# Performance work log

Measured on AMD Instinct MI355X. Metric: run time of the kernel, lower is better.

Reference implementation:

```python
import jax, jax.numpy as jnp
import numpy as np

EPS = 1e-5
DIM_HEAD = 64
HEADS = 8

def layernorm(x, gamma, beta):
    mu = jnp.mean(x, axis=-1, keepdims=True)
    var = jnp.var(x, axis=-1, keepdims=True)
    return (x - mu) * jax.lax.rsqrt(var + EPS) * gamma + beta

def setup_inputs() -> dict:
    key = jax.random.key(0)
    ks = jax.random.split(key, 8)
    b, n, dh = 1, 896, 3072       # batch, enformer seq len, enformer_hidden_dim
    c, j, dc = 64, 127, 1024      # num contexts (tracks), context len, context_dim
    inner = HEADS * DIM_HEAD      # 512
    return {
        "embeddings": jax.random.normal(ks[0], (b, n, dh), jnp.float32),
        "context": jax.random.normal(ks[1], (c, j, dc), jnp.float32),
        "context_mask": jax.random.randint(ks[2], (b, j), 0, 2) > 0,
        "q_gamma": jnp.ones((dh,), jnp.float32),
        "q_beta": jnp.zeros((dh,), jnp.float32),
        "kv_gamma": jnp.ones((dc,), jnp.float32),
        "kv_beta": jnp.zeros((dc,), jnp.float32),
        "Wq": jax.random.normal(ks[3], (dh, inner), jnp.float32) * 0.02,
        "Wkv": jax.random.normal(ks[4], (dc, 2 * inner), jnp.float32) * 0.02,
        "null_k": jax.random.normal(ks[5], (inner,), jnp.float32),
        "null_v": jax.random.normal(ks[6], (inner,), jnp.float32),
        "Wo": jax.random.normal(ks[7], (inner, dh), jnp.float32) * 0.02,
        "bo": jnp.zeros((dh,), jnp.float32),
        "Wp": jax.random.normal(jax.random.fold_in(key, 9), (dh, 1), jnp.float32) * 0.02,
        "bp": jnp.zeros((1,), jnp.float32),
    }

def reference(embeddings, context, context_mask, q_gamma, q_beta, kv_gamma, kv_beta,
              Wq, Wkv, null_k, null_v, Wo, bo, Wp, bp):
    h, d = HEADS, DIM_HEAD
    scale = d ** -0.5
    b, n, dh = embeddings.shape
    c = context.shape[0]
    # projections
    q = layernorm(embeddings, q_gamma, q_beta) @ Wq            # (b, n, h*d)
    kv = layernorm(context, kv_gamma, kv_beta) @ Wkv           # (c, j, 2*h*d)
    k, v = jnp.split(kv, 2, axis=-1)
    # prepend null key/value token
    k = jnp.concatenate([jnp.broadcast_to(null_k, (c, 1, h * d)), k], axis=1)
    v = jnp.concatenate([jnp.broadcast_to(null_v, (c, 1, h * d)), v], axis=1)
    # split heads: (b, h, i, d) / (c, h, j, d)
    q = q.reshape(b, n, h, d).transpose(0, 2, 1, 3)
    k = k.reshape(c, -1, h, d).transpose(0, 2, 1, 3)
    v = v.reshape(c, -1, h, d).transpose(0, 2, 1, 3)
    sim = jnp.einsum('bhid,chjd->bchij', q, k) * scale         # (b, c, h, i, j+1)
    # mask: pad with True for the null token, broadcast over c, h, i
    mask = jnp.pad(context_mask, ((0, 0), (1, 0)), constant_values=True)
    sim = jnp.where(mask[:, None, None, None, :], sim, -jnp.finfo(sim.dtype).max)
    attn = jax.nn.softmax(sim, axis=-1)
    out = jnp.einsum('bchij,chjd->bchid', attn, v)             # (b, c, h, i, d)
    out = out.transpose(0, 1, 3, 2, 4).reshape(b, c, n, h * d)  # (b, c, n, h*d)
    branch = out @ Wo + bo                                     # (b, c, n, dh)
    emb = embeddings[:, None] + branch                         # (b, c, n, dh)
    pred = jax.nn.softplus((emb @ Wp + bp)[..., 0])            # (b, c, n)
    return pred.transpose(0, 2, 1)                             # (b, n, c)
```

## Files before the change

kernel.cpp:

```cpp
#include <hip/hip_runtime.h>
#include <math.h>

#define N_SEQ   896
#define DH      3072
#define NCTX    64
#define JLEN    127
#define DC      1024
#define HEADS   8
#define DHEAD   64
#define INNER   512
#define MKV     8128
#define MKVPAD  8192

typedef __bf16 bf16x8 __attribute__((ext_vector_type(8)));
typedef float  f32x4  __attribute__((ext_vector_type(4)));

#define OFF_EDOT   0LL
#define OFF_QBF    (OFF_EDOT + N_SEQ)
#define OFF_KBF    (OFF_QBF  + (long long)N_SEQ*INNER/2)
#define OFF_VPM    (OFF_KBF  + (long long)NCTX*128*INNER/2)
#define OFF_VPNULL (OFF_VPM  + (long long)MKV*8)
#define OFF_WOP    (OFF_VPNULL + 8)
#define OFF_BOP    (OFF_WOP  + INNER)
#define OFF_SBUF   (OFF_BOP  + 16)
#define OFF_ANQ    (OFF_SBUF + (long long)NCTX*HEADS*N_SEQ)
#define OFF_ANKV   (OFF_ANQ  + (long long)N_SEQ*DH/2)
#define OFF_WQT    (OFF_ANKV + (long long)MKVPAD*DC/2)
#define OFF_WKT    (OFF_WQT  + (long long)INNER*DH/2)
#define OFF_WVPT   (OFF_WKT  + (long long)INNER*DC/2)
#define OFF_QSL    (OFF_WVPT + 16*1024/2)

__device__ __forceinline__ void async_copy16(const __bf16* g, __bf16* l) {
    __builtin_amdgcn_global_load_lds(
        (const __attribute__((address_space(1))) unsigned int*)g,
        (__attribute__((address_space(3))) unsigned int*)l,
        16, 0, 0);
}

template <int P>
__device__ __forceinline__
void ln_row(const float* __restrict__ x,
            const float* __restrict__ gamma, const float* __restrict__ beta,
            const float* __restrict__ wp,
            __bf16* __restrict__ o, float* __restrict__ dotout) {
    const int K = P * 1024;
    float4 xv[P];
    float s = 0.f, ss = 0.f, dp = 0.f;
    #pragma unroll
    for (int p = 0; p < P; ++p) {
        xv[p] = *(const float4*)&x[p * 1024 + threadIdx.x * 4];
        s  += xv[p].x + xv[p].y + xv[p].z + xv[p].w;
        ss += xv[p].x * xv[p].x + xv[p].y * xv[p].y
            + xv[p].z * xv[p].z + xv[p].w * xv[p].w;
        if (wp) {
            float4 w4 = *(const float4*)&wp[p * 1024 + threadIdx.x * 4];
            dp += xv[p].x * w4.x + xv[p].y * w4.y + xv[p].z * w4.z + xv[p].w * w4.w;
        }
    }
    #pragma unroll
    for (int ofs = 32; ofs > 0; ofs >>= 1) {
        s  += __shfl_down(s,  ofs);
        ss += __shfl_down(ss, ofs);
        dp += __shfl_down(dp, ofs);
    }
    __shared__ float red[3][4];
    __shared__ float sh_mu, sh_rstd;
    int lane = threadIdx.x & 63, w = threadIdx.x >> 6;
    if (lane == 0) { red[0][w] = s; red[1][w] = ss; red[2][w] = dp; }
    __syncthreads();
    if (threadIdx.x == 0) {
        float S  = red[0][0] + red[0][1] + red[0][2] + red[0][3];
        float SS = red[1][0] + red[1][1] + red[1][2] + red[1][3];
        float m = S / K;
        sh_mu = m;
        sh_rstd = rsqrtf(SS / K - m * m + 1e-5f);
        if (dotout) *dotout = red[2][0] + red[2][1] + red[2][2] + red[2][3];
    }
    __syncthreads();
    float m = sh_mu, r = sh_rstd;
    #pragma unroll
    for (int p = 0; p < P; ++p) {
        int col = p * 1024 + threadIdx.x * 4;
        float4 g4 = *(const float4*)&gamma[col];
        float4 b4 = *(const float4*)&beta[col];
        __bf16 ov[4];
        ov[0] = (__bf16)((xv[p].x - m) * r * g4.x + b4.x);
        ov[1] = (__bf16)((xv[p].y - m) * r * g4.y + b4.y);
        ov[2] = (__bf16)((xv[p].z - m) * r * g4.z + b4.z);
        ov[3] = (__bf16)((xv[p].w - m) * r * g4.w + b4.w);
        *(ushort4*)&o[col] = *(ushort4*)ov;
    }
}

__global__ __launch_bounds__(256)
void ln_wop_kernel(const float* __restrict__ emb, const float* __restrict__ ctx,
                   const float* __restrict__ qg, const float* __restrict__ qb,
                   const float* __restrict__ kvg, const float* __restrict__ kvb,
                   const float* __restrict__ Wp, const float* __restrict__ Wo,
                   const float* __restrict__ bo,
                   __bf16* __restrict__ anq, __bf16* __restrict__ ankv,
                   float* __restrict__ edot, float* __restrict__ wop,
                   float* __restrict__ bop) {
    int b = blockIdx.x;
    if (b < N_SEQ) {
        ln_row<3>(emb + (long long)b * DH, qg, qb, Wp,
                  anq + (long long)b * DH, edot + b);
    } else if (b < N_SEQ + MKV) {
        int r = b - N_SEQ;
        ln_row<1>(ctx + (long long)r * DC, kvg, kvb, nullptr,
                  ankv + (long long)r * DC, nullptr);
    } else {
        int r = b - (N_SEQ + MKV);
        const float* src = (r < INNER) ? (Wo + (long long)r * DH) : bo;
        float s = 0.f;
        for (int k = threadIdx.x; k < DH; k += 256) s += src[k] * Wp[k];
        #pragma unroll
        for (int o = 32; o > 0; o >>= 1) s += __shfl_down(s, o);
        __shared__ float red2[4];
        int lane = threadIdx.x & 63, w = threadIdx.x >> 6;
        if (lane == 0) red2[w] = s;
        __syncthreads();
        if (threadIdx.x == 0) {
            float S = red2[0] + red2[1] + red2[2] + red2[3];
            if (r < INNER) wop[r] = S; else *bop = S;
        }
    }
}

__device__ __forceinline__
void transpose_tile(const float* __restrict__ src, int srcStride,
                    __bf16* __restrict__ dst, int dstStride,
                    int rb, int cb, float t[32][33]) {
    int tx = threadIdx.x & 31, ty = threadIdx.x >> 5;
    #pragma unroll
    for (int i = 0; i < 32; i += 8)
        t[ty + i][tx] = src[(long long)(rb + ty + i) * srcStride + cb + tx];
    __syncthreads();
    #pragma unroll
    for (int i = 0; i < 32; i += 8)
        dst[(long long)(cb + ty + i) * dstStride + rb + tx] = (__bf16)t[tx][ty + i];
}

__global__ __launch_bounds__(256)
void prep2_kernel(const float* __restrict__ Wq, const float* __restrict__ Wkv,
                  const float* __restrict__ wop,
                  const float* __restrict__ null_v, const float* __restrict__ null_k,
                  __bf16* __restrict__ wqt, __bf16* __restrict__ wkt,
                  __bf16* __restrict__ wvpt, float* __restrict__ vpnull,
                  __bf16* __restrict__ k_bf) {
    __shared__ float t[32][33];
    int b = blockIdx.x;
    if (b < 1536) {
        int rb = (b >> 4) * 32, cb = (b & 15) * 32;
        transpose_tile(Wq, INNER, wqt, DH, rb, cb, t);
    } else if (b < 2048) {
        int bi = b - 1536;
        int rb = (bi >> 4) * 32, cb = (bi & 15) * 32;
        transpose_tile(Wkv, 2 * INNER, wkt, DC, rb, cb, t);
    } else if (b < 2080) {
        int tt = (b - 2048) * 256 + threadIdx.x;
        int k = tt >> 3, h = tt & 7;
        const float* src = Wkv + (long long)k * (2 * INNER) + INNER + h * 64;
        const float* wv  = wop + h * 64;
        float s = 0.f;
        #pragma unroll 16
        for (int d = 0; d < 64; ++d) s += src[d] * wv[d];
        wvpt[h * 1024 + k] = (__bf16)s;
    } else {
        for (int i = threadIdx.x; i < 8 * 1024; i += 256)
            wvpt[8 * 1024 + i] = (__bf16)0.f;
        for (int i = threadIdx.x; i < NCTX * INNER; i += 256) {
            int c = i >> 9, d = i & 511;
            k_bf[(long long)(c * 128) * INNER + d] = (__bf16)null_k[d];
        }
        if (threadIdx.x < 8) {
            int h = threadIdx.x;
            float s = 0.f;
            #pragma unroll 16
            for (int d = 0; d < 64; ++d) s += null_v[h * 64 + d] * wop[h * 64 + d];
            vpnull[h] = s;
        }
    }
}

__global__ __launch_bounds__(256)
void proj_kernel(const __bf16* __restrict__ ANQ, const __bf16* __restrict__ WQT,
                 const __bf16* __restrict__ ANKV, const __bf16* __restrict__ WKT,
                 const __bf16* __restrict__ WVPT,
                 float* __restrict__ qsl, __bf16* __restrict__ kout,
                 float* __restrict__ vpm) {
    __shared__ __align__(16) __bf16 As[128 * 32];
    __shared__ __align__(16) __bf16 Bs[128 * 32];
    int b = blockIdx.x;
    int tid = threadIdx.x;
    int lane = tid & 63, w = tid >> 6;
    int n16 = lane & 15, quad = lane >> 4;
    int wr = (w >> 1) * 64, wc = (w & 1) * 64;

    const __bf16 *A, *B;
    int K, kbeg, kend, mode, slice = 0;
    long long m0, n0;
    if (b < 224) {
        mode = 0; slice = b / 28;
        int rem = b % 28;
        m0 = (long long)(rem % 7) * 128;
        n0 = (long long)(rem / 7) * 128;
        K = DH; kbeg = slice * 384; kend = kbeg + 384;
        A = ANQ; B = WQT;
    } else {
        mode = 1;
        int b2 = b - 224;
        m0 = (long long)(b2 & 63) * 128;
        n0 = (long long)(b2 >> 6) * 128;
        K = DC; kbeg = 0; kend = DC;
        A = ANKV; B = WKT;
    }
    bool dovp = (mode == 1) && (n0 == 0);

    const __bf16* aG = A + (m0 + (tid >> 2)) * K + (tid & 3) * 8;
    const __bf16* bG = B + (n0 + (tid >> 2)) * K + (tid & 3) * 8;
    __bf16* aL = As + tid * 8;
    __bf16* bL = Bs + tid * 8;

    f32x4 acc[4][4], accv[4];
    const f32x4 z = {0.f, 0.f, 0.f, 0.f};
    #pragma unroll
    for (int i = 0; i < 4; ++i) {
        accv[i] = z;
        #pragma unroll
        for (int j = 0; j < 4; ++j) acc[i][j] = z;
    }

    for (int k0 = kbeg; k0 < kend; k0 += 32) {
        async_copy16(aG + k0, aL);
        async_copy16(aG + (long long)64 * K + k0, aL + 2048);
        async_copy16(bG + k0, bL);
        async_copy16(bG + (long long)64 * K + k0, bL + 2048);
        bf16x8 bv;
        if (dovp) bv = *(const bf16x8*)&WVPT[n16 * 1024 + k0 + quad * 8];
        __syncthreads();
        bf16x8 af[4], bfr[4];
        #pragma unroll
        for (int i = 0; i < 4; ++i)
            af[i]  = *(const bf16x8*)&As[(wr + i * 16 + n16) * 32 + quad * 8];
        #pragma unroll
        for (int j = 0; j < 4; ++j)
            bfr[j] = *(const bf16x8*)&Bs[(wc + j * 16 + n16) * 32 + quad * 8];
        #pragma unroll
        for (int i = 0; i < 4; ++i)
            #pragma unroll
            for (int j = 0; j < 4; ++j)
                acc[i][j] = __builtin_amdgcn_mfma_f32_16x16x32_bf16(af[i], bfr[j], acc[i][j], 0, 0, 0);
        if (dovp) {
            #pragma unroll
            for (int i = 0; i < 4; ++i)
                accv[i] = __builtin_amdgcn_mfma_f32_16x16x32_bf16(af[i], bv, accv[i], 0, 0, 0);
        }
        __syncthreads();
    }

    if (mode == 0) {
        float* qdst = qsl + (long long)slice * (N_SEQ * INNER);
        #pragma unroll
        for (int i = 0; i < 4; ++i)
            #pragma unroll
            for (int r = 0; r < 4; ++r) {
                long long gr = m0 + wr + i * 16 + quad * 4 + r;
                #pragma unroll
                for (int j = 0; j < 4; ++j) {
                    long long gc = n0 + wc + j * 16 + n16;
                    qdst[gr * INNER + gc] = acc[i][j][r];
                }
            }
    } else {
        #pragma unroll
        for (int i = 0; i < 4; ++i)
            #pragma unroll
            for (int r = 0; r < 4; ++r) {
                long long gr = m0 + wr + i * 16 + quad * 4 + r;
                if (gr >= MKV) continue;
                int cc = (int)(gr / JLEN), jj = (int)(gr % JLEN);
                #pragma unroll
                for (int j = 0; j < 4; ++j) {
                    long long gc = n0 + wc + j * 16 + n16;
                    kout[((long long)(cc * 128) + jj + 1) * INNER + gc] = (__bf16)acc[i][j][r];
                }
                if (dovp && n16 < 8) vpm[gr * 8 + n16] = accv[i][r];
            }
    }
}

__global__ void qreduce_kernel(const float* __restrict__ qsl, __bf16* __restrict__ qbf) {
    int t = blockIdx.x * 256 + threadIdx.x;
    float s = 0.f;
    #pragma unroll
    for (int k = 0; k < 8; ++k) s += qsl[(long long)k * (N_SEQ * INNER) + t];
    qbf[t] = (__bf16)s;
}

#define KROW 72

__global__ __launch_bounds__(256)
void attn_mfma_kernel(const __bf16* __restrict__ qb, const __bf16* __restrict__ kb,
                      const float* __restrict__ vpm, const float* __restrict__ vpnull,
                      const int* __restrict__ mask, float* __restrict__ s_buf) {
    __shared__ __align__(16) __bf16 ksh[128 * KROW];
    __shared__ float vpsh[128];
    __shared__ float amsh[128];
    int ch = blockIdx.y;
    int h = ch & 7, c = ch >> 3;
    int tid = threadIdx.x;
    int lane = tid & 63, w = tid >> 6;
    int n16 = lane & 15, quad = lane >> 4;

    const __bf16* kbase = kb + (long long)(c * 128) * INNER + h * DHEAD;
    #pragma unroll
    for (int p = 0; p < 4; ++p) {
        int chunk = tid + p * 256;
        int row = chunk >> 3, o = chunk & 7;
        bf16x8 v = *(const bf16x8*)(kbase + (long long)row * INNER + o * 8);
        *(bf16x8*)&ksh[row * KROW + o * 8] = v;
    }
    if (tid < 128) {
        vpsh[tid] = (tid == 0) ? vpnull[h] : vpm[(long long)(c * JLEN + tid - 1) * 8 + h];
        amsh[tid] = (tid == 0) ? 0.f : (mask[tid - 1] ? 0.f : -3.0e38f);
    }
    __syncthreads();

    bf16x8 bF[8][2];
    #pragma unroll
    for (int t = 0; t < 8; ++t)
        #pragma unroll
        for (int s = 0; s < 2; ++s)
            bF[t][s] = *(const bf16x8*)&ksh[(t * 16 + n16) * KROW + s * 32 + quad * 8];

    float vpv[8], am[8];
    #pragma unroll
    for (int t = 0; t < 8; ++t) {
        vpv[t] = vpsh[t * 16 + n16];
        am[t]  = amsh[t * 16 + n16];
    }

    const __bf16* qbase = qb + h * DHEAD;
    bf16x8 aF[2][2];
    int r0s[2];
    #pragma unroll
    for (int it2 = 0; it2 < 2; ++it2) {
        int tile = blockIdx.x * 8 + it2 * 4 + w;
        r0s[it2] = tile * 16;
        const __bf16* qrow = qbase + (long long)(r0s[it2] + n16) * INNER + quad * 8;
        aF[it2][0] = *(const bf16x8*)(qrow);
        aF[it2][1] = *(const bf16x8*)(qrow + 32);
    }

    const f32x4 zero = {0.f, 0.f, 0.f, 0.f};
    #pragma unroll
    for (int it2 = 0; it2 < 2; ++it2) {
        int r0 = r0s[it2];
        f32x4 acc[8];
        #pragma unroll
        for (int t = 0; t < 8; ++t) {
            acc[t] = __builtin_amdgcn_mfma_f32_16x16x32_bf16(aF[it2][0], bF[t][0], zero,   0, 0, 0);
            acc[t] = __builtin_amdgcn_mfma_f32_16x16x32_bf16(aF[it2][1], bF[t][1], acc[t], 0, 0, 0);
        }
        float mloc = -3.0e38f;
        #pragma unroll
        for (int t = 0; t < 8; ++t)
            #pragma unroll
            for (int r = 0; r < 4; ++r)
                mloc = fmaxf(mloc, acc[t][r] * 0.125f + am[t]);
        #pragma unroll
        for (int o = 1; o < 16; o <<= 1) mloc = fmaxf(mloc, __shfl_xor(mloc, o, 16));
        float lr[4] = {0.f, 0.f, 0.f, 0.f}, pr[4] = {0.f, 0.f, 0.f, 0.f};
        #pragma unroll
        for (int t = 0; t < 8; ++t) {
            #pragma unroll
            for (int r = 0; r < 4; ++r) {
                float e = __expf(acc[t][r] * 0.125f + am[t] - mloc);
                lr[r] += e; pr[r] += e * vpv[t];
            }
        }
        #pragma unroll
        for (int o = 1; o < 16; o <<= 1) {
            #pragma unroll
            for (int r = 0; r < 4; ++r) {
                lr[r] += __shfl_xor(lr[r], o, 16);
                pr[r] += __shfl_xor(pr[r], o, 16);
            }
        }
        if (n16 == 0) {
            #pragma unroll
            for (int r = 0; r < 4; ++r)
                s_buf[(long long)ch * N_SEQ + r0 + quad * 4 + r] = pr[r] / lr[r];
        }
    }
}

__global__ void final_kernel(const float* __restrict__ s_buf,
                             const float* __restrict__ e_dot,
                             const float* __restrict__ bop,
                             const float* __restrict__ bp,
                             float* __restrict__ out) {
    int t = blockIdx.x * blockDim.x + threadIdx.x;
    if (t >= N_SEQ * NCTX) return;
    int n = t >> 6, c = t & 63;
    float s = 0.f;
    #pragma unroll
    for (int h = 0; h < HEADS; ++h) s += s_buf[((long long)(c * HEADS + h)) * N_SEQ + n];
    float x = e_dot[n] + s + *bop + *bp;
    out[t] = fmaxf(x, 0.f) + log1pf(__expf(-fabsf(x)));
}

extern "C" void kernel_launch(void* const* d_in, const int* in_sizes, int n_in,
                              void* d_out, int out_size, void* d_ws, size_t ws_size,
                              hipStream_t stream) {
    const float* emb   = (const float*)d_in[0];
    const float* ctx   = (const float*)d_in[1];
    const int*   cmask = (const int*)  d_in[2];
    const float* qg    = (const float*)d_in[3];
    const float* qb_   = (const float*)d_in[4];
    const float* kvg   = (const float*)d_in[5];
    const float* kvb   = (const float*)d_in[6];
    const float* Wq    = (const float*)d_in[7];
    const float* Wkv   = (const float*)d_in[8];
    const float* nullk = (const float*)d_in[9];
    const float* nullv = (const float*)d_in[10];
    const float* Wo    = (const float*)d_in[11];
    const float* bo    = (const float*)d_in[12];
    const float* Wp    = (const float*)d_in[13];
    const float* bp    = (const float*)d_in[14];
    float* out  = (float*)d_out;
    float* ws_f = (float*)d_ws;

    float*  EDOT   = ws_f + OFF_EDOT;
    __bf16* QBF    = (__bf16*)(ws_f + OFF_QBF);
    __bf16* KBF    = (__bf16*)(ws_f + OFF_KBF);
    float*  VPM    = ws_f + OFF_VPM;
    float*  VPNULL = ws_f + OFF_VPNULL;
    float*  WOP    = ws_f + OFF_WOP;
    float*  BOP    = ws_f + OFF_BOP;
    float*  SBUF   = ws_f + OFF_SBUF;
    __bf16* ANQ    = (__bf16*)(ws_f + OFF_ANQ);
    __bf16* ANKV   = (__bf16*)(ws_f + OFF_ANKV);
    __bf16* WQT    = (__bf16*)(ws_f + OFF_WQT);
    __bf16* WKT    = (__bf16*)(ws_f + OFF_WKT);
    __bf16* WVPT   = (__bf16*)(ws_f + OFF_WVPT);
    float*  QSL    = ws_f + OFF_QSL;

    ln_wop_kernel<<<N_SEQ + MKV + INNER + 1, 256, 0, stream>>>(
        emb, ctx, qg, qb_, kvg, kvb, Wp, Wo, bo, ANQ, ANKV, EDOT, WOP, BOP);
    prep2_kernel<<<2081, 256, 0, stream>>>(
        Wq, Wkv, WOP, nullv, nullk, WQT, WKT, WVPT, VPNULL, KBF);
    proj_kernel<<<480, 256, 0, stream>>>(ANQ, WQT, ANKV, WKT, WVPT, QSL, KBF, VPM);
    qreduce_kernel<<<(N_SEQ * INNER) / 256, 256, 0, stream>>>(QSL, QBF);
    attn_mfma_kernel<<<dim3(7, NCTX * HEADS), 256, 0, stream>>>(
        QBF, KBF, VPM, VPNULL, cmask, SBUF);
    final_kernel<<<(N_SEQ * NCTX + 255) / 256, 256, 0, stream>>>(SBUF, EDOT, BOP, bp, out);
}
```

Before: 216.1 us.

## Fuse all stages into one cooperative persistent kernel with grid syncs

Replaces the six-kernel pipeline (layernorm, weight prep, projection GEMM, q-reduce, attention, final softplus) with a single cooperative kernel whose blocks loop over each stage's work and separate stages with grid-wide barriers. The layernorm becomes one wave per row instead of one block per row, and the Wo·Wp fold is merged into the per-head value-projection work. The aim is to remove kernel launch gaps and tail idle time between stages. In exchange, grid size is capped by occupancy, so some stages run with fewer concurrent blocks, and each grid sync costs time of its own.

```diff
diff --git a/kernel.cpp b/kernel.cpp
--- a/kernel.cpp
+++ b/kernel.cpp
@@ -1,5 +1,8 @@
 #include <hip/hip_runtime.h>
+#include <hip/hip_cooperative_groups.h>
 #include <math.h>
+
+namespace cg = cooperative_groups;
 
 #define N_SEQ   896
 #define DH      3072
@@ -37,378 +40,417 @@
         16, 0, 0);
 }
 
-template <int P>
-__device__ __forceinline__
-void ln_row(const float* __restrict__ x,
-            const float* __restrict__ gamma, const float* __restrict__ beta,
-            const float* __restrict__ wp,
-            __bf16* __restrict__ o, float* __restrict__ dotout) {
-    const int K = P * 1024;
-    float4 xv[P];
-    float s = 0.f, ss = 0.f, dp = 0.f;
-    #pragma unroll
-    for (int p = 0; p < P; ++p) {
-        xv[p] = *(const float4*)&x[p * 1024 + threadIdx.x * 4];
-        s  += xv[p].x + xv[p].y + xv[p].z + xv[p].w;
-        ss += xv[p].x * xv[p].x + xv[p].y * xv[p].y
-            + xv[p].z * xv[p].z + xv[p].w * xv[p].w;
-        if (wp) {
-            float4 w4 = *(const float4*)&wp[p * 1024 + threadIdx.x * 4];
-            dp += xv[p].x * w4.x + xv[p].y * w4.y + xv[p].z * w4.z + xv[p].w * w4.w;
-        }
-    }
-    #pragma unroll
-    for (int ofs = 32; ofs > 0; ofs >>= 1) {
-        s  += __shfl_down(s,  ofs);
-        ss += __shfl_down(ss, ofs);
-        dp += __shfl_down(dp, ofs);
-    }
-    __shared__ float red[3][4];
-    __shared__ float sh_mu, sh_rstd;
-    int lane = threadIdx.x & 63, w = threadIdx.x >> 6;
-    if (lane == 0) { red[0][w] = s; red[1][w] = ss; red[2][w] = dp; }
-    __syncthreads();
-    if (threadIdx.x == 0) {
-        float S  = red[0][0] + red[0][1] + red[0][2] + red[0][3];
-        float SS = red[1][0] + red[1][1] + red[1][2] + red[1][3];
-        float m = S / K;
-        sh_mu = m;
-        sh_rstd = rsqrtf(SS / K - m * m + 1e-5f);
-        if (dotout) *dotout = red[2][0] + red[2][1] + red[2][2] + red[2][3];
-    }
-    __syncthreads();
-    float m = sh_mu, r = sh_rstd;
-    #pragma unroll
-    for (int p = 0; p < P; ++p) {
-        int col = p * 1024 + threadIdx.x * 4;
-        float4 g4 = *(const float4*)&gamma[col];
-        float4 b4 = *(const float4*)&beta[col];
-        __bf16 ov[4];
-        ov[0] = (__bf16)((xv[p].x - m) * r * g4.x + b4.x);
-        ov[1] = (__bf16)((xv[p].y - m) * r * g4.y + b4.y);
-        ov[2] = (__bf16)((xv[p].z - m) * r * g4.z + b4.z);
-        ov[3] = (__bf16)((xv[p].w - m) * r * g4.w + b4.w);
-        *(ushort4*)&o[col] = *(ushort4*)ov;
-    }
-}
-
-__global__ __launch_bounds__(256)
-void ln_wop_kernel(const float* __restrict__ emb, const float* __restrict__ ctx,
-                   const float* __restrict__ qg, const float* __restrict__ qb,
-                   const float* __restrict__ kvg, const float* __restrict__ kvb,
-                   const float* __restrict__ Wp, const float* __restrict__ Wo,
-                   const float* __restrict__ bo,
-                   __bf16* __restrict__ anq, __bf16* __restrict__ ankv,
-                   float* __restrict__ edot, float* __restrict__ wop,
-                   float* __restrict__ bop) {
-    int b = blockIdx.x;
-    if (b < N_SEQ) {
-        ln_row<3>(emb + (long long)b * DH, qg, qb, Wp,
-                  anq + (long long)b * DH, edot + b);
-    } else if (b < N_SEQ + MKV) {
-        int r = b - N_SEQ;
-        ln_row<1>(ctx + (long long)r * DC, kvg, kvb, nullptr,
-                  ankv + (long long)r * DC, nullptr);
-    } else {
-        int r = b - (N_SEQ + MKV);
-        const float* src = (r < INNER) ? (Wo + (long long)r * DH) : bo;
-        float s = 0.f;
-        for (int k = threadIdx.x; k < DH; k += 256) s += src[k] * Wp[k];
-        #pragma unroll
-        for (int o = 32; o > 0; o >>= 1) s += __shfl_down(s, o);
-        __shared__ float red2[4];
-        int lane = threadIdx.x & 63, w = threadIdx.x >> 6;
-        if (lane == 0) red2[w] = s;
-        __syncthreads();
-        if (threadIdx.x == 0) {
-            float S = red2[0] + red2[1] + red2[2] + red2[3];
-            if (r < INNER) wop[r] = S; else *bop = S;
-        }
-    }
-}
-
-__device__ __forceinline__
-void transpose_tile(const float* __restrict__ src, int srcStride,
-                    __bf16* __restrict__ dst, int dstStride,
-                    int rb, int cb, float t[32][33]) {
-    int tx = threadIdx.x & 31, ty = threadIdx.x >> 5;
-    #pragma unroll
-    for (int i = 0; i < 32; i += 8)
-        t[ty + i][tx] = src[(long long)(rb + ty + i) * srcStride + cb + tx];
-    __syncthreads();
-    #pragma unroll
-    for (int i = 0; i < 32; i += 8)
-        dst[(long long)(cb + ty + i) * dstStride + rb + tx] = (__bf16)t[tx][ty + i];
-}
-
-__global__ __launch_bounds__(256)
-void prep2_kernel(const float* __restrict__ Wq, const float* __restrict__ Wkv,
-                  const float* __restrict__ wop,
-                  const float* __restrict__ null_v, const float* __restrict__ null_k,
-                  __bf16* __restrict__ wqt, __bf16* __restrict__ wkt,
-                  __bf16* __restrict__ wvpt, float* __restrict__ vpnull,
-                  __bf16* __restrict__ k_bf) {
-    __shared__ float t[32][33];
-    int b = blockIdx.x;
-    if (b < 1536) {
-        int rb = (b >> 4) * 32, cb = (b & 15) * 32;
-        transpose_tile(Wq, INNER, wqt, DH, rb, cb, t);
-    } else if (b < 2048) {
-        int bi = b - 1536;
-        int rb = (bi >> 4) * 32, cb = (bi & 15) * 32;
-        transpose_tile(Wkv, 2 * INNER, wkt, DC, rb, cb, t);
-    } else if (b < 2080) {
-        int tt = (b - 2048) * 256 + threadIdx.x;
-        int k = tt >> 3, h = tt & 7;
-        const float* src = Wkv + (long long)k * (2 * INNER) + INNER + h * 64;
-        const float* wv  = wop + h * 64;
-        float s = 0.f;
-        #pragma unroll 16
-        for (int d = 0; d < 64; ++d) s += src[d] * wv[d];
-        wvpt[h * 1024 + k] = (__bf16)s;
-    } else {
-        for (int i = threadIdx.x; i < 8 * 1024; i += 256)
-            wvpt[8 * 1024 + i] = (__bf16)0.f;
-        for (int i = threadIdx.x; i < NCTX * INNER; i += 256) {
-            int c = i >> 9, d = i & 511;
-            k_bf[(long long)(c * 128) * INNER + d] = (__bf16)null_k[d];
-        }
-        if (threadIdx.x < 8) {
-            int h = threadIdx.x;
+#define KROW 72
+
+__global__ __launch_bounds__(256, 2)
+void mega_kernel(const float* __restrict__ emb, const float* __restrict__ ctx,
+                 const int* __restrict__ cmask,
+                 const float* __restrict__ qg, const float* __restrict__ qb_,
+                 const float* __restrict__ kvg, const float* __restrict__ kvb,
+                 const float* __restrict__ Wq, const float* __restrict__ Wkv,
+                 const float* __restrict__ nullk, const float* __restrict__ nullv,
+                 const float* __restrict__ Wo, const float* __restrict__ bo,
+                 const float* __restrict__ Wp, const float* __restrict__ bp,
+                 float* __restrict__ out, float* __restrict__ ws_f)
+{
+    __shared__ __align__(16) unsigned char SMEM[19456];
+    cg::grid_group gg = cg::this_grid();
+
+    float*  EDOT   = ws_f + OFF_EDOT;
+    __bf16* QBF    = (__bf16*)(ws_f + OFF_QBF);
+    __bf16* KBF    = (__bf16*)(ws_f + OFF_KBF);
+    float*  VPM    = ws_f + OFF_VPM;
+    float*  VPNULL = ws_f + OFF_VPNULL;
+    float*  BOP    = ws_f + OFF_BOP;
+    float*  SBUF   = ws_f + OFF_SBUF;
+    __bf16* ANQ    = (__bf16*)(ws_f + OFF_ANQ);
+    __bf16* ANKV   = (__bf16*)(ws_f + OFF_ANKV);
+    __bf16* WQT    = (__bf16*)(ws_f + OFF_WQT);
+    __bf16* WKT    = (__bf16*)(ws_f + OFF_WKT);
+    __bf16* WVPT   = (__bf16*)(ws_f + OFF_WVPT);
+    float*  QSL    = ws_f + OFF_QSL;
+
+    const int NB   = gridDim.x;
+    const int bid  = blockIdx.x;
+    const int tid  = threadIdx.x;
+    const int lane = tid & 63;
+    const int wid  = tid >> 6;
+
+    {
+        const int gw = bid * 4 + wid, NW = NB * 4;
+        for (int r = gw; r < MKV; r += NW) {
+            const float* x = ctx + (long long)r * DC;
+            float4 xv[4];
+            float s = 0.f, ss = 0.f;
+            #pragma unroll
+            for (int c = 0; c < 4; ++c) {
+                xv[c] = *(const float4*)&x[c * 256 + lane * 4];
+                s  += xv[c].x + xv[c].y + xv[c].z + xv[c].w;
+                ss += xv[c].x*xv[c].x + xv[c].y*xv[c].y + xv[c].z*xv[c].z + xv[c].w*xv[c].w;
+            }
+            #pragma unroll
+            for (int o = 1; o < 64; o <<= 1) { s += __shfl_xor(s, o); ss += __shfl_xor(ss, o); }
+            float m = s * (1.f / DC);
+            float rs = rsqrtf(ss * (1.f / DC) - m * m + 1e-5f);
+            __bf16* op = ANKV + (long long)r * DC;
+            #pragma unroll
+            for (int c = 0; c < 4; ++c) {
+                int col = c * 256 + lane * 4;
+                float4 g4 = *(const float4*)&kvg[col];
+                float4 b4 = *(const float4*)&kvb[col];
+                __bf16 ov[4];
+                ov[0] = (__bf16)((xv[c].x - m) * rs * g4.x + b4.x);
+                ov[1] = (__bf16)((xv[c].y - m) * rs * g4.y + b4.y);
+                ov[2] = (__bf16)((xv[c].z - m) * rs * g4.z + b4.z);
+                ov[3] = (__bf16)((xv[c].w - m) * rs * g4.w + b4.w);
+                *(ushort4*)&op[col] = *(ushort4*)ov;
+            }
+        }
+        for (int r = gw; r < N_SEQ; r += NW) {
+            const float* x = emb + (long long)r * DH;
+            float4 xv[12];
+            float s = 0.f, ss = 0.f, dp = 0.f;
+            #pragma unroll
+            for (int c = 0; c < 12; ++c) {
+                int col = c * 256 + lane * 4;
+                xv[c] = *(const float4*)&x[col];
+                float4 w4 = *(const float4*)&Wp[col];
+                s  += xv[c].x + xv[c].y + xv[c].z + xv[c].w;
+                ss += xv[c].x*xv[c].x + xv[c].y*xv[c].y + xv[c].z*xv[c].z + xv[c].w*xv[c].w;
+                dp += xv[c].x*w4.x + xv[c].y*w4.y + xv[c].z*w4.z + xv[c].w*w4.w;
+            }
+            #pragma unroll
+            for (int o = 1; o < 64; o <<= 1) {
+                s += __shfl_xor(s, o); ss += __shfl_xor(ss, o); dp += __shfl_xor(dp, o);
+            }
+            float m = s * (1.f / DH);
+            float rs = rsqrtf(ss * (1.f / DH) - m * m + 1e-5f);
+            __bf16* op = ANQ + (long long)r * DH;
+            #pragma unroll
+            for (int c = 0; c < 12; ++c) {
+                int col = c * 256 + lane * 4;
+                float4 g4 = *(const float4*)&qg[col];
+                float4 b4 = *(const float4*)&qb_[col];
+                __bf16 ov[4];
+                ov[0] = (__bf16)((xv[c].x - m) * rs * g4.x + b4.x);
+                ov[1] = (__bf16)((xv[c].y - m) * rs * g4.y + b4.y);
+                ov[2] = (__bf16)((xv[c].z - m) * rs * g4.z + b4.z);
+                ov[3] = (__bf16)((xv[c].w - m) * rs * g4.w + b4.w);
+                *(ushort4*)&op[col] = *(ushort4*)ov;
+            }
+            if (lane == 0) EDOT[r] = dp;
+        }
+    }
+
+    {
+        float (*tT)[33] = (float(*)[33])SMEM;
+        for (int t = bid; t < 2058; t += NB) {
+            if (t < 2048) {
+                const float* src; __bf16* dst; int srcS, dstS, rb, cb;
+                if (t < 1536) {
+                    rb = (t >> 4) * 32; cb = (t & 15) * 32;
+                    src = Wq; srcS = INNER; dst = WQT; dstS = DH;
+                } else {
+                    int bi = t - 1536;
+                    rb = (bi >> 4) * 32; cb = (bi & 15) * 32;
+                    src = Wkv; srcS = 2 * INNER; dst = WKT; dstS = DC;
+                }
+                int tx = tid & 31, ty = tid >> 5;
+                __syncthreads();
+                #pragma unroll
+                for (int i = 0; i < 32; i += 8)
+                    tT[ty + i][tx] = src[(long long)(rb + ty + i) * srcS + cb + tx];
+                __syncthreads();
+                #pragma unroll
+                for (int i = 0; i < 32; i += 8)
+                    dst[(long long)(cb + ty + i) * dstS + rb + tx] = (__bf16)tT[tx][ty + i];
+            } else if (t < 2056) {
+                int h = t - 2048;
+                float* wops = (float*)SMEM;
+                __syncthreads();
+                int d = tid >> 2, part = tid & 3;
+                const float* worow = Wo + (long long)(h * 64 + d) * DH;
+                float s = 0.f;
+                for (int k = part * 4; k < DH; k += 16) {
+                    float4 a = *(const float4*)&worow[k];
+                    float4 w = *(const float4*)&Wp[k];
+                    s += a.x*w.x + a.y*w.y + a.z*w.z + a.w*w.w;
+                }
+                s += __shfl_xor(s, 1); s += __shfl_xor(s, 2);
+                if (part == 0) wops[d] = s;
+                __syncthreads();
+                if (tid < 64) {
+                    float v = nullv[h * 64 + tid] * wops[tid];
+                    #pragma unroll
+                    for (int o = 1; o < 64; o <<= 1) v += __shfl_xor(v, o);
+                    if (tid == 0) VPNULL[h] = v;
+                }
+                for (int k = tid; k < 1024; k += 256) {
+                    const float* src = Wkv + (long long)k * (2 * INNER) + INNER + h * 64;
+                    float s2 = 0.f;
+                    #pragma unroll
+                    for (int d2 = 0; d2 < 64; d2 += 4) {
+                        float4 a = *(const float4*)&src[d2];
+                        s2 += a.x*wops[d2] + a.y*wops[d2+1] + a.z*wops[d2+2] + a.w*wops[d2+3];
+                    }
+                    WVPT[h * 1024 + k] = (__bf16)s2;
+                }
+            } else if (t == 2056) {
+                float* red = (float*)SMEM;
+                __syncthreads();
+                float s = 0.f;
+                #pragma unroll
+                for (int i = 0; i < 3; ++i) {
+                    int k = i * 1024 + tid * 4;
+                    float4 a = *(const float4*)&bo[k];
+                    float4 w = *(const float4*)&Wp[k];
+                    s += a.x*w.x + a.y*w.y + a.z*w.z + a.w*w.w;
+                }
+                #pragma unroll
+                for (int o = 1; o < 64; o <<= 1) s += __shfl_xor(s, o);
+                if (lane == 0) red[wid] = s;
+                __syncthreads();
+                if (tid == 0) *BOP = red[0] + red[1] + red[2] + red[3];
+            } else {
+                for (int i = tid; i < 8 * 1024; i += 256)
+                    WVPT[8 * 1024 + i] = (__bf16)0.f;
+                for (int i = tid; i < NCTX * INNER; i += 256) {
+                    int c = i >> 9, d2 = i & 511;
+                    KBF[(long long)(c * 128) * INNER + d2] = (__bf16)nullk[d2];
+                }
+            }
+        }
+    }
+
+    gg.sync();
+
+    {
+        __bf16* As = (__bf16*)SMEM;
+        __bf16* Bs = As + 128 * 32;
+        for (int b = bid; b < 480; b += NB) {
+            int n16 = lane & 15, quad = lane >> 4;
+            int wr = (wid >> 1) * 64, wc = (wid & 1) * 64;
+
+            const __bf16 *A, *B;
+            int K, kbeg, kend, mode, slice = 0;
+            long long m0, n0;
+            if (b < 224) {
+                mode = 0; slice = b / 28;
+                int rem = b % 28;
+                m0 = (long long)(rem % 7) * 128;
+                n0 = (long long)(rem / 7) * 128;
+                K = DH; kbeg = slice * 384; kend = kbeg + 384;
+                A = ANQ; B = WQT;
+            } else {
+                mode = 1;
+                int b2 = b - 224;
+                m0 = (long long)(b2 & 63) * 128;
+                n0 = (long long)(b2 >> 6) * 128;
+                K = DC; kbeg = 0; kend = DC;
+                A = ANKV; B = WKT;
+            }
+            bool dovp = (mode == 1) && (n0 == 0);
+
+            const __bf16* aG = A + (m0 + (tid >> 2)) * K + (tid & 3) * 8;
+            const __bf16* bG = B + (n0 + (tid >> 2)) * K + (tid & 3) * 8;
+            __bf16* aL = As + tid * 8;
+            __bf16* bL = Bs + tid * 8;
+
+            f32x4 acc[4][4], accv[4];
+            const f32x4 z = {0.f, 0.f, 0.f, 0.f};
+            #pragma unroll
+            for (int i = 0; i < 4; ++i) {
+                accv[i] = z;
+                #pragma unroll
+                for (int j = 0; j < 4; ++j) acc[i][j] = z;
+            }
+
+            for (int k0 = kbeg; k0 < kend; k0 += 32) {
+                async_copy16(aG + k0, aL);
+                async_copy16(aG + (long long)64 * K + k0, aL + 2048);
+                async_copy16(bG + k0, bL);
+                async_copy16(bG + (long long)64 * K + k0, bL + 2048);
+                bf16x8 bv;
+                if (dovp) bv = *(const bf16x8*)&WVPT[n16 * 1024 + k0 + quad * 8];
+                __syncthreads();
+                bf16x8 af[4], bfr[4];
+                #pragma unroll
+                for (int i = 0; i < 4; ++i)
+                    af[i]  = *(const bf16x8*)&As[(wr + i * 16 + n16) * 32 + quad * 8];
+                #pragma unroll
+                for (int j = 0; j < 4; ++j)
+                    bfr[j] = *(const bf16x8*)&Bs[(wc + j * 16 + n16) * 32 + quad * 8];
+                #pragma unroll
+                for (int i = 0; i < 4; ++i)
+                    #pragma unroll
+                    for (int j = 0; j < 4; ++j)
+                        acc[i][j] = __builtin_amdgcn_mfma_f32_16x16x32_bf16(af[i], bfr[j], acc[i][j], 0, 0, 0);
+                if (dovp) {
+                    #pragma unroll
+                    for (int i = 0; i < 4; ++i)
+                        accv[i] = __builtin_amdgcn_mfma_f32_16x16x32_bf16(af[i], bv, accv[i], 0, 0, 0);
+                }
+                __syncthreads();
+            }
+
+            if (mode == 0) {
+                float* qdst = QSL + (long long)slice * (N_SEQ * INNER);
+                #pragma unroll
+                for (int i = 0; i < 4; ++i)
+                    #pragma unroll
+                    for (int r = 0; r < 4; ++r) {
+                        long long gr = m0 + wr + i * 16 + quad * 4 + r;
+                        #pragma unroll
+                        for (int j = 0; j < 4; ++j) {
+                            long long gc = n0 + wc + j * 16 + n16;
+                            qdst[gr * INNER + gc] = acc[i][j][r];
+                        }
+                    }
+            } else {
+                #pragma unroll
+                for (int i = 0; i < 4; ++i)
+                    #pragma unroll
+                    for (int r = 0; r < 4; ++r) {
+                        long long gr = m0 + wr + i * 16 + quad * 4 + r;
+                        if (gr >= MKV) continue;
+                        int cc = (int)(gr / JLEN), jj = (int)(gr % JLEN);
+                        #pragma unroll
+                        for (int j = 0; j < 4; ++j) {
+                            long long gc = n0 + wc + j * 16 + n16;
+                            KBF[((long long)(cc * 128) + jj + 1) * INNER + gc] = (__bf16)acc[i][j][r];
+                        }
+                        if (dovp && n16 < 8) VPM[gr * 8 + n16] = accv[i][r];
+                    }
+            }
+        }
+    }
+
+    gg.sync();
+
+    {
+        const int gt = bid * 256 + tid, NT = NB * 256;
+        for (int i = gt; i < (N_SEQ * INNER) / 4; i += NT) {
+            float4 s4 = {0.f, 0.f, 0.f, 0.f};
+            #pragma unroll
+            for (int k = 0; k < 8; ++k) {
+                float4 a = *(const float4*)&QSL[(long long)k * (N_SEQ * INNER) + i * 4];
+                s4.x += a.x; s4.y += a.y; s4.z += a.z; s4.w += a.w;
+            }
+            __bf16 ov[4] = {(__bf16)s4.x, (__bf16)s4.y, (__bf16)s4.z, (__bf16)s4.w};
+            *(ushort4*)&QBF[i * 4] = *(ushort4*)ov;
+        }
+    }
+
+    gg.sync();
+
+    {
+        __bf16* ksh  = (__bf16*)SMEM;
+        float*  vpsh = (float*)(SMEM + 18432);
+        float*  amsh = (float*)(SMEM + 18944);
+        for (int t = bid; t < 3584; t += NB) {
+            int ch = t & 511, qx = t >> 9;
+            int h = ch & 7, c = ch >> 3;
+            int n16 = lane & 15, quad = lane >> 4;
+
+            __syncthreads();
+            const __bf16* kbase = KBF + (long long)(c * 128) * INNER + h * DHEAD;
+            #pragma unroll
+            for (int p = 0; p < 4; ++p) {
+                int chunk = tid + p * 256;
+                int row = chunk >> 3, o = chunk & 7;
+                bf16x8 v = *(const bf16x8*)(kbase + (long long)row * INNER + o * 8);
+                *(bf16x8*)&ksh[row * KROW + o * 8] = v;
+            }
+            if (tid < 128) {
+                vpsh[tid] = (tid == 0) ? VPNULL[h] : VPM[(long long)(c * JLEN + tid - 1) * 8 + h];
+                amsh[tid] = (tid == 0) ? 0.f : (cmask[tid - 1] ? 0.f : -3.0e38f);
+            }
+            __syncthreads();
+
+            bf16x8 bF[8][2];
+            #pragma unroll
+            for (int tt = 0; tt < 8; ++tt)
+                #pragma unroll
+                for (int s = 0; s < 2; ++s)
+                    bF[tt][s] = *(const bf16x8*)&ksh[(tt * 16 + n16) * KROW + s * 32 + quad * 8];
+
+            float vpv[8], am[8];
+            #pragma unroll
+            for (int tt = 0; tt < 8; ++tt) {
+                vpv[tt] = vpsh[tt * 16 + n16];
+                am[tt]  = amsh[tt * 16 + n16];
+            }
+
+            const __bf16* qbase = QBF + h * DHEAD;
+            bf16x8 aF[2][2];
+            int r0s[2];
+            #pragma unroll
+            for (int it2 = 0; it2 < 2; ++it2) {
+                int tile = qx * 8 + it2 * 4 + wid;
+                r0s[it2] = tile * 16;
+                const __bf16* qrow = qbase + (long long)(r0s[it2] + n16) * INNER + quad * 8;
+                aF[it2][0] = *(const bf16x8*)(qrow);
+                aF[it2][1] = *(const bf16x8*)(qrow + 32);
+            }
+
+            const f32x4 zero = {0.f, 0.f, 0.f, 0.f};
+            #pragma unroll
+            for (int it2 = 0; it2 < 2; ++it2) {
+                int r0 = r0s[it2];
+                f32x4 acc[8];
+                #pragma unroll
+                for (int tt = 0; tt < 8; ++tt) {
+                    acc[tt] = __builtin_amdgcn_mfma_f32_16x16x32_bf16(aF[it2][0], bF[tt][0], zero,    0, 0, 0);
+                    acc[tt] = __builtin_amdgcn_mfma_f32_16x16x32_bf16(aF[it2][1], bF[tt][1], acc[tt], 0, 0, 0);
+                }
+                float mloc = -3.0e38f;
+                #pragma unroll
+                for (int tt = 0; tt < 8; ++tt)
+                    #pragma unroll
+                    for (int r = 0; r < 4; ++r)
+                        mloc = fmaxf(mloc, acc[tt][r] * 0.125f + am[tt]);
+                #pragma unroll
+                for (int o = 1; o < 16; o <<= 1) mloc = fmaxf(mloc, __shfl_xor(mloc, o, 16));
+                float lr[4] = {0.f, 0.f, 0.f, 0.f}, pr[4] = {0.f, 0.f, 0.f, 0.f};
+                #pragma unroll
+                for (int tt = 0; tt < 8; ++tt) {
+                    #pragma unroll
+                    for (int r = 0; r < 4; ++r) {
+                        float e = __expf(acc[tt][r] * 0.125f + am[tt] - mloc);
+                        lr[r] += e; pr[r] += e * vpv[tt];
+                    }
+                }
+                #pragma unroll
+                for (int o = 1; o < 16; o <<= 1) {
+                    #pragma unroll
+                    for (int r = 0; r < 4; ++r) {
+                        lr[r] += __shfl_xor(lr[r], o, 16);
+                        pr[r] += __shfl_xor(pr[r], o, 16);
+                    }
+                }
+                if (n16 == 0) {
+                    #pragma unroll
+                    for (int r = 0; r < 4; ++r)
+                        SBUF[(long long)ch * N_SEQ + r0 + quad * 4 + r] = pr[r] / lr[r];
+                }
+            }
+        }
+    }
+
+    gg.sync();
+
+    {
+        const int gt = bid * 256 + tid, NT = NB * 256;
+        float bsum = *BOP + *bp;
+        for (int i = gt; i < N_SEQ * NCTX; i += NT) {
+            int n = i >> 6, c = i & 63;
             float s = 0.f;
-            #pragma unroll 16
-            for (int d = 0; d < 64; ++d) s += null_v[h * 64 + d] * wop[h * 64 + d];
-            vpnull[h] = s;
-        }
-    }
-}
-
-__global__ __launch_bounds__(256)
-void proj_kernel(const __bf16* __restrict__ ANQ, const __bf16* __restrict__ WQT,
-                 const __bf16* __restrict__ ANKV, const __bf16* __restrict__ WKT,
-                 const __bf16* __restrict__ WVPT,
-                 float* __restrict__ qsl, __bf16* __restrict__ kout,
-                 float* __restrict__ vpm) {
-    __shared__ __align__(16) __bf16 As[128 * 32];
-    __shared__ __align__(16) __bf16 Bs[128 * 32];
-    int b = blockIdx.x;
-    int tid = threadIdx.x;
-    int lane = tid & 63, w = tid >> 6;
-    int n16 = lane & 15, quad = lane >> 4;
-    int wr = (w >> 1) * 64, wc = (w & 1) * 64;
-
-    const __bf16 *A, *B;
-    int K, kbeg, kend, mode, slice = 0;
-    long long m0, n0;
-    if (b < 224) {
-        mode = 0; slice = b / 28;
-        int rem = b % 28;
-        m0 = (long long)(rem % 7) * 128;
-        n0 = (long long)(rem / 7) * 128;
-        K = DH; kbeg = slice * 384; kend = kbeg + 384;
-        A = ANQ; B = WQT;
-    } else {
-        mode = 1;
-        int b2 = b - 224;
-        m0 = (long long)(b2 & 63) * 128;
-        n0 = (long long)(b2 >> 6) * 128;
-        K = DC; kbeg = 0; kend = DC;
-        A = ANKV; B = WKT;
-    }
-    bool dovp = (mode == 1) && (n0 == 0);
-
-    const __bf16* aG = A + (m0 + (tid >> 2)) * K + (tid & 3) * 8;
-    const __bf16* bG = B + (n0 + (tid >> 2)) * K + (tid & 3) * 8;
-    __bf16* aL = As + tid * 8;
-    __bf16* bL = Bs + tid * 8;
-
-    f32x4 acc[4][4], accv[4];
-    const f32x4 z = {0.f, 0.f, 0.f, 0.f};
-    #pragma unroll
-    for (int i = 0; i < 4; ++i) {
-        accv[i] = z;
-        #pragma unroll
-        for (int j = 0; j < 4; ++j) acc[i][j] = z;
-    }
-
-    for (int k0 = kbeg; k0 < kend; k0 += 32) {
-        async_copy16(aG + k0, aL);
-        async_copy16(aG + (long long)64 * K + k0, aL + 2048);
-        async_copy16(bG + k0, bL);
-        async_copy16(bG + (long long)64 * K + k0, bL + 2048);
-        bf16x8 bv;
-        if (dovp) bv = *(const bf16x8*)&WVPT[n16 * 1024 + k0 + quad * 8];
-        __syncthreads();
-        bf16x8 af[4], bfr[4];
-        #pragma unroll
-        for (int i = 0; i < 4; ++i)
-            af[i]  = *(const bf16x8*)&As[(wr + i * 16 + n16) * 32 + quad * 8];
-        #pragma unroll
-        for (int j = 0; j < 4; ++j)
-            bfr[j] = *(const bf16x8*)&Bs[(wc + j * 16 + n16) * 32 + quad * 8];
-        #pragma unroll
-        for (int i = 0; i < 4; ++i)
-            #pragma unroll
-            for (int j = 0; j < 4; ++j)
-                acc[i][j] = __builtin_amdgcn_mfma_f32_16x16x32_bf16(af[i], bfr[j], acc[i][j], 0, 0, 0);
-        if (dovp) {
-            #pragma unroll
-            for (int i = 0; i < 4; ++i)
-                accv[i] = __builtin_amdgcn_mfma_f32_16x16x32_bf16(af[i], bv, accv[i], 0, 0, 0);
-        }
-        __syncthreads();
-    }
-
-    if (mode == 0) {
-        float* qdst = qsl + (long long)slice * (N_SEQ * INNER);
-        #pragma unroll
-        for (int i = 0; i < 4; ++i)
-            #pragma unroll
-            for (int r = 0; r < 4; ++r) {
-                long long gr = m0 + wr + i * 16 + quad * 4 + r;
-                #pragma unroll
-                for (int j = 0; j < 4; ++j) {
-                    long long gc = n0 + wc + j * 16 + n16;
-                    qdst[gr * INNER + gc] = acc[i][j][r];
-                }
-            }
-    } else {
-        #pragma unroll
-        for (int i = 0; i < 4; ++i)
-            #pragma unroll
-            for (int r = 0; r < 4; ++r) {
-                long long gr = m0 + wr + i * 16 + quad * 4 + r;
-                if (gr >= MKV) continue;
-                int cc = (int)(gr / JLEN), jj = (int)(gr % JLEN);
-                #pragma unroll
-                for (int j = 0; j < 4; ++j) {
-                    long long gc = n0 + wc + j * 16 + n16;
-                    kout[((long long)(cc * 128) + jj + 1) * INNER + gc] = (__bf16)acc[i][j][r];
-                }
-                if (dovp && n16 < 8) vpm[gr * 8 + n16] = accv[i][r];
-            }
-    }
-}
-
-__global__ void qreduce_kernel(const float* __restrict__ qsl, __bf16* __restrict__ qbf) {
-    int t = blockIdx.x * 256 + threadIdx.x;
-    float s = 0.f;
-    #pragma unroll
-    for (int k = 0; k < 8; ++k) s += qsl[(long long)k * (N_SEQ * INNER) + t];
-    qbf[t] = (__bf16)s;
-}
-
-#define KROW 72
-
-__global__ __launch_bounds__(256)
-void attn_mfma_kernel(const __bf16* __restrict__ qb, const __bf16* __restrict__ kb,
-                      const float* __restrict__ vpm, const float* __restrict__ vpnull,
-                      const int* __restrict__ mask, float* __restrict__ s_buf) {
-    __shared__ __align__(16) __bf16 ksh[128 * KROW];
-    __shared__ float vpsh[128];
-    __shared__ float amsh[128];
-    int ch = blockIdx.y;
-    int h = ch & 7, c = ch >> 3;
-    int tid = threadIdx.x;
-    int lane = tid & 63, w = tid >> 6;
-    int n16 = lane & 15, quad = lane >> 4;
-
-    const __bf16* kbase = kb + (long long)(c * 128) * INNER + h * DHEAD;
-    #pragma unroll
-    for (int p = 0; p < 4; ++p) {
-        int chunk = tid + p * 256;
-        int row = chunk >> 3, o = chunk & 7;
-        bf16x8 v = *(const bf16x8*)(kbase + (long long)row * INNER + o * 8);
-        *(bf16x8*)&ksh[row * KROW + o * 8] = v;
-    }
-    if (tid < 128) {
-        vpsh[tid] = (tid == 0) ? vpnull[h] : vpm[(long long)(c * JLEN + tid - 1) * 8 + h];
-        amsh[tid] = (tid == 0) ? 0.f : (mask[tid - 1] ? 0.f : -3.0e38f);
-    }
-    __syncthreads();
-
-    bf16x8 bF[8][2];
-    #pragma unroll
-    for (int t = 0; t < 8; ++t)
-        #pragma unroll
-        for (int s = 0; s < 2; ++s)
-            bF[t][s] = *(const bf16x8*)&ksh[(t * 16 + n16) * KROW + s * 32 + quad * 8];
-
-    float vpv[8], am[8];
-    #pragma unroll
-    for (int t = 0; t < 8; ++t) {
-        vpv[t] = vpsh[t * 16 + n16];
-        am[t]  = amsh[t * 16 + n16];
-    }
-
-    const __bf16* qbase = qb + h * DHEAD;
-    bf16x8 aF[2][2];
-    int r0s[2];
-    #pragma unroll
-    for (int it2 = 0; it2 < 2; ++it2) {
-        int tile = blockIdx.x * 8 + it2 * 4 + w;
-        r0s[it2] = tile * 16;
-        const __bf16* qrow = qbase + (long long)(r0s[it2] + n16) * INNER + quad * 8;
-        aF[it2][0] = *(const bf16x8*)(qrow);
-        aF[it2][1] = *(const bf16x8*)(qrow + 32);
-    }
-
-    const f32x4 zero = {0.f, 0.f, 0.f, 0.f};
-    #pragma unroll
-    for (int it2 = 0; it2 < 2; ++it2) {
-        int r0 = r0s[it2];
-        f32x4 acc[8];
-        #pragma unroll
-        for (int t = 0; t < 8; ++t) {
-            acc[t] = __builtin_amdgcn_mfma_f32_16x16x32_bf16(aF[it2][0], bF[t][0], zero,   0, 0, 0);
-            acc[t] = __builtin_amdgcn_mfma_f32_16x16x32_bf16(aF[it2][1], bF[t][1], acc[t], 0, 0, 0);
-        }
-        float mloc = -3.0e38f;
-        #pragma unroll
-        for (int t = 0; t < 8; ++t)
-            #pragma unroll
-            for (int r = 0; r < 4; ++r)
-                mloc = fmaxf(mloc, acc[t][r] * 0.125f + am[t]);
-        #pragma unroll
-        for (int o = 1; o < 16; o <<= 1) mloc = fmaxf(mloc, __shfl_xor(mloc, o, 16));
-        float lr[4] = {0.f, 0.f, 0.f, 0.f}, pr[4] = {0.f, 0.f, 0.f, 0.f};
-        #pragma unroll
-        for (int t = 0; t < 8; ++t) {
-            #pragma unroll
-            for (int r = 0; r < 4; ++r) {
-                float e = __expf(acc[t][r] * 0.125f + am[t] - mloc);
-                lr[r] += e; pr[r] += e * vpv[t];
-            }
-        }
-        #pragma unroll
-        for (int o = 1; o < 16; o <<= 1) {
-            #pragma unroll
-            for (int r = 0; r < 4; ++r) {
-                lr[r] += __shfl_xor(lr[r], o, 16);
-                pr[r] += __shfl_xor(pr[r], o, 16);
-            }
-        }
-        if (n16 == 0) {
-            #pragma unroll
-            for (int r = 0; r < 4; ++r)
-                s_buf[(long long)ch * N_SEQ + r0 + quad * 4 + r] = pr[r] / lr[r];
-        }
-    }
-}
-
-__global__ void final_kernel(const float* __restrict__ s_buf,
-                             const float* __restrict__ e_dot,
-                             const float* __restrict__ bop,
-                             const float* __restrict__ bp,
-                             float* __restrict__ out) {
-    int t = blockIdx.x * blockDim.x + threadIdx.x;
-    if (t >= N_SEQ * NCTX) return;
-    int n = t >> 6, c = t & 63;
-    float s = 0.f;
-    #pragma unroll
-    for (int h = 0; h < HEADS; ++h) s += s_buf[((long long)(c * HEADS + h)) * N_SEQ + n];
-    float x = e_dot[n] + s + *bop + *bp;
-    out[t] = fmaxf(x, 0.f) + log1pf(__expf(-fabsf(x)));
+            #pragma unroll
+            for (int h = 0; h < HEADS; ++h) s += SBUF[((long long)(c * HEADS + h)) * N_SEQ + n];
+            float x = EDOT[n] + s + bsum;
+            out[i] = fmaxf(x, 0.f) + log1pf(__expf(-fabsf(x)));
+        }
+    }
 }
 
 extern "C" void kernel_launch(void* const* d_in, const int* in_sizes, int n_in,
@@ -432,28 +474,23 @@
     float* out  = (float*)d_out;
     float* ws_f = (float*)d_ws;
 
-    float*  EDOT   = ws_f + OFF_EDOT;
-    __bf16* QBF    = (__bf16*)(ws_f + OFF_QBF);
-    __bf16* KBF    = (__bf16*)(ws_f + OFF_KBF);
-    float*  VPM    = ws_f + OFF_VPM;
-    float*  VPNULL = ws_f + OFF_VPNULL;
-    float*  WOP    = ws_f + OFF_WOP;
-    float*  BOP    = ws_f + OFF_BOP;
-    float*  SBUF   = ws_f + OFF_SBUF;
-    __bf16* ANQ    = (__bf16*)(ws_f + OFF_ANQ);
-    __bf16* ANKV   = (__bf16*)(ws_f + OFF_ANKV);
-    __bf16* WQT    = (__bf16*)(ws_f + OFF_WQT);
-    __bf16* WKT    = (__bf16*)(ws_f + OFF_WKT);
-    __bf16* WVPT   = (__bf16*)(ws_f + OFF_WVPT);
-    float*  QSL    = ws_f + OFF_QSL;
-
-    ln_wop_kernel<<<N_SEQ + MKV + INNER + 1, 256, 0, stream>>>(
-        emb, ctx, qg, qb_, kvg, kvb, Wp, Wo, bo, ANQ, ANKV, EDOT, WOP, BOP);
-    prep2_kernel<<<2081, 256, 0, stream>>>(
-        Wq, Wkv, WOP, nullv, nullk, WQT, WKT, WVPT, VPNULL, KBF);
-    proj_kernel<<<480, 256, 0, stream>>>(ANQ, WQT, ANKV, WKT, WVPT, QSL, KBF, VPM);
-    qreduce_kernel<<<(N_SEQ * INNER) / 256, 256, 0, stream>>>(QSL, QBF);
-    attn_mfma_kernel<<<dim3(7, NCTX * HEADS), 256, 0, stream>>>(
-        QBF, KBF, VPM, VPNULL, cmask, SBUF);
-    final_kernel<<<(N_SEQ * NCTX + 255) / 256, 256, 0, stream>>>(SBUF, EDOT, BOP, bp, out);
+    static int nblk = 0;
+    if (nblk == 0) {
+        int maxb = 0;
+        if (hipOccupancyMaxActiveBlocksPerMultiprocessor(&maxb, mega_kernel, 256, 0) != hipSuccess
+            || maxb < 1) maxb = 2;
+        long long g = (long long)maxb * 256;
+        if (g > 1024) g = 1024;
+        if (g < 256)  g = 256;
+        nblk = (int)g;
+    }
+
+    void* kargs[] = {
+        (void*)&emb, (void*)&ctx, (void*)&cmask, (void*)&qg, (void*)&qb_,
+        (void*)&kvg, (void*)&kvb, (void*)&Wq, (void*)&Wkv, (void*)&nullk,
+        (void*)&nullv, (void*)&Wo, (void*)&bo, (void*)&Wp, (void*)&bp,
+        (void*)&out, (void*)&ws_f
+    };
+    hipLaunchCooperativeKernel((const void*)mega_kernel, dim3(nblk), dim3(256),
+                               kargs, 0, stream);
 }
```

Measured after the change: 432.3 us. +100.0%, slower.
